# Optimization experiments

Measured on AMD Instinct MI355X. Metric: run time of the kernel, lower is better.

Reference implementation:

```python
import jax, jax.numpy as jnp
import numpy as np

S_SIGMA = 8      # spatial downsampling of the bilateral grid
N_BINS = 16      # intensity bins (range resolution)
EPS = 1e-8


def _blur_axis(g, k, axis):
    """1D correlation of grid g with small tap filter k along `axis` (zero pad)."""
    taps = k.shape[0]
    r = taps // 2
    pad = [(0, 0)] * g.ndim
    pad[axis] = (r, r)
    gp = jnp.pad(g, pad)
    n = g.shape[axis]
    out = k[0] * jax.lax.slice_in_dim(gp, 0, n, axis=axis)
    for i in range(1, taps):
        out = out + k[i] * jax.lax.slice_in_dim(gp, i, i + n, axis=axis)
    return out


def _bilateral_one(img, fs, fr):
    """Bilateral grid splat -> blur -> slice for a single [H,W] channel.
    Guide signal is the channel itself (values assumed in [0,1])."""
    H, W = img.shape
    GH = (H - 1) // S_SIGMA + 2
    GW = (W - 1) // S_SIGMA + 2
    GZ = N_BINS + 1

    ys = jnp.arange(H, dtype=img.dtype)
    xs = jnp.arange(W, dtype=img.dtype)

    # ---- splat (nearest-cell scatter-add of homogeneous (value, weight)) ----
    gy = jnp.round(ys / S_SIGMA).astype(jnp.int32)            # [H]
    gx = jnp.round(xs / S_SIGMA).astype(jnp.int32)            # [W]
    gyg, gxg = jnp.meshgrid(gy, gx, indexing='ij')            # [H,W]
    gz = jnp.clip(jnp.round(img * (N_BINS - 1)), 0, N_BINS - 1).astype(jnp.int32)
    val = jnp.zeros((GH, GW, GZ), img.dtype).at[gyg, gxg, gz].add(img)
    wt = jnp.zeros((GH, GW, GZ), img.dtype).at[gyg, gxg, gz].add(jnp.ones_like(img))

    # ---- blur grid: learnable 5-tap filter_s along y,x and filter_r along z ----
    for axis, k in ((0, fs), (1, fs), (2, fr)):
        val = _blur_axis(val, k, axis)
        wt = _blur_axis(wt, k, axis)

    # ---- slice (trilinear gather at (y/s, x/s, I*(NB-1))) ----
    fy = ys / S_SIGMA
    fx = xs / S_SIGMA
    fz = jnp.clip(img * (N_BINS - 1), 0.0, N_BINS - 1)        # [H,W]
    y0 = jnp.floor(fy).astype(jnp.int32)
    x0 = jnp.floor(fx).astype(jnp.int32)
    z0 = jnp.floor(fz).astype(jnp.int32)
    y1 = jnp.minimum(y0 + 1, GH - 1)
    x1 = jnp.minimum(x0 + 1, GW - 1)
    z1 = jnp.minimum(z0 + 1, GZ - 1)
    ty = fy - y0.astype(img.dtype)                            # [H]
    tx = fx - x0.astype(img.dtype)                            # [W]
    tz = fz - z0.astype(img.dtype)                            # [H,W]

    out_v = jnp.zeros_like(img)
    out_w = jnp.zeros_like(img)
    for yi, wy in ((y0, 1.0 - ty), (y1, ty)):
        for xi, wx in ((x0, 1.0 - tx), (x1, tx)):
            for zi, wz in ((z0, 1.0 - tz), (z1, tz)):
                w = wy[:, None] * wx[None, :] * wz            # [H,W]
                out_v = out_v + w * val[yi[:, None], xi[None, :], zi]
                out_w = out_w + w * wt[yi[:, None], xi[None, :], zi]
    return out_v / (out_w + EPS)


def setup_inputs() -> dict:
    key = jax.random.key(0)
    k1, k2 = jax.random.split(key)
    blurred_batch = jax.random.uniform(k1, (4, 3, 1024, 1024), dtype=jnp.float32)
    kernel_batch = jax.random.uniform(k2, (4, 11, 11), dtype=jnp.float32)
    g = jnp.array([1.0, 4.0, 6.0, 4.0, 1.0], dtype=jnp.float32)
    g = g / g.sum()  # smooth 5-tap filter so the blur is nontrivial
    return {
        'blurred_batch': blurred_batch,
        'kernel_batch': kernel_batch,
        'filter_s': g,
        'filter_r': g,
        'num_irls_iter': 1,
        'num_cg_iter': 5,
    }


def reference(blurred_batch, kernel_batch, filter_s, filter_r, num_irls_iter, num_cg_iter):
    # kernel_batch, num_irls_iter, num_cg_iter are unused on this code path,
    # matching the original forward (only BilateralGrid.apply touches x).
    B, C, H, W = blurred_batch.shape
    imgs = blurred_batch.reshape(B * C, H, W)
    out = jax.vmap(lambda im: _bilateral_one(im, filter_s, filter_r))(imgs)
    return out.reshape(B, C, H, W)
```

## Files before the change

kernel.cpp:

```cpp
#include <hip/hip_runtime.h>

#define S_SIGMA 8
#define NBINS   16
#define HDIM    1024
#define WDIM    1024
#define GH      129
#define GW      129
#define GZ      17
#define CELLS   (GH*GW*GZ)
#define ROWSZ   (GW*GZ)
#define EPSV    1e-8f
#define FIXS    1048576.0f
#define FIXI    (1.0f/1048576.0f)

__global__ __launch_bounds__(256) void splat_gather_kernel(
    const float* __restrict__ img, float* __restrict__ grid, int nImg, int imgBase)
{
    __shared__ unsigned lval[16 * 64];
    __shared__ unsigned lwt [16 * 64];

    int tid = threadIdx.x;
    int c   = tid & 63;
    int q   = tid >> 6;
    int cellIdx = blockIdx.x * 64 + c;
    int total = nImg * GH * GW;

    for (int i = tid; i < 16 * 64; i += 256) { lval[i] = 0u; lwt[i] = 0u; }
    __syncthreads();

    if (cellIdx < total) {
        int b   = cellIdx / (GH * GW);
        int rem = cellIdx - b * (GH * GW);
        int gy  = rem / GW;
        int gx  = rem - gy * GW;
        const float* ib = img + (size_t)(imgBase + b) * (HDIM * WDIM);

        bool interior = (gx >= 1) & (gx <= 127) & (gy >= 1) & (gy <= 127);
        if (interior) {
            int py = gy & 1, px = gx & 1;
            int ylo = 8 * gy - 4 + py;
            int nr  = 9 - 2 * py;
            int ax  = 8 * gx - 4;
            for (int r = q; r < nr; r += 4) {
                const float* rp = ib + (size_t)(ylo + r) * WDIM + ax;
                float4 A = *(const float4*)rp;
                float4 B = *(const float4*)(rp + 4);
                float  cv = rp[8];
                float e7[7] = {A.y, A.z, A.w, B.x, B.y, B.z, B.w};
                #pragma unroll
                for (int j = 0; j < 7; ++j) {
                    float v = e7[j];
                    int gz = min(max((int)rintf(v * 15.0f), 0), 15);
                    atomicAdd(&lval[gz * 64 + c], (unsigned)rintf(v * FIXS));
                    atomicAdd(&lwt [gz * 64 + c], 1u);
                }
                if (!px) {
                    int gz = min(max((int)rintf(A.x * 15.0f), 0), 15);
                    atomicAdd(&lval[gz * 64 + c], (unsigned)rintf(A.x * FIXS));
                    atomicAdd(&lwt [gz * 64 + c], 1u);
                    gz = min(max((int)rintf(cv * 15.0f), 0), 15);
                    atomicAdd(&lval[gz * 64 + c], (unsigned)rintf(cv * FIXS));
                    atomicAdd(&lwt [gz * 64 + c], 1u);
                }
            }
        } else {
            int ylo = max(0, 8 * gy - 4 + (gy & 1));
            int yhi = min(HDIM - 1, 8 * gy + 4 - (gy & 1));
            int xlo = max(0, 8 * gx - 4 + (gx & 1));
            int xhi = min(WDIM - 1, 8 * gx + 4 - (gx & 1));
            for (int y = ylo + q; y <= yhi; y += 4) {
                const float* row = ib + (size_t)y * WDIM;
                for (int x = xlo; x <= xhi; ++x) {
                    float v = row[x];
                    int gz = min(max((int)rintf(v * 15.0f), 0), 15);
                    atomicAdd(&lval[gz * 64 + c], (unsigned)rintf(v * FIXS));
                    atomicAdd(&lwt [gz * 64 + c], 1u);
                }
            }
        }
    }
    __syncthreads();

    if (cellIdx < total) {
        float2* dst = (float2*)grid + (size_t)cellIdx * GZ;
        int zlo = q * 4;
        int zhi = (q == 3) ? 17 : zlo + 4;
        for (int z = zlo; z < zhi; ++z) {
            float2 o;
            if (z == 16) { o.x = 0.f; o.y = 0.f; }
            else {
                o.x = (float)lval[z * 64 + c] * FIXI;
                o.y = (float)lwt [z * 64 + c];
            }
            dst[z] = o;
        }
    }
}

#define TO 12
#define TI 16
#define NIN  (TI*TI*GZ)
#define NTMP (TO*TI*GZ)
#define NOUT (TO*TO*GZ)
#define NTI  13
#define NXI  10

__global__ __launch_bounds__(256) void blur_fused_kernel(
    const float2* __restrict__ in, float2* __restrict__ out,
    const float* __restrict__ kfs, const float* __restrict__ kfr)
{
    __shared__ float2 sbin[NIN];

    int tid = threadIdx.x;
    int tx0 = blockIdx.x * TO;
    int ty0 = blockIdx.y * TO;
    int b   = blockIdx.z;

    float ks[5] = {kfs[0], kfs[1], kfs[2], kfs[3], kfs[4]};
    float kr[5] = {kfr[0], kfr[1], kfr[2], kfr[3], kfr[4]};

    const float2* gb = in + (size_t)b * CELLS;
    for (int li = tid; li < NIN; li += 256) {
        int iy = li / (TI * GZ);
        int r  = li - iy * (TI * GZ);
        int ix = r / GZ;
        int z  = r - ix * GZ;
        int gy = ty0 - 2 + iy;
        int gx = tx0 - 2 + ix;
        float2 v; v.x = 0.f; v.y = 0.f;
        if (gy >= 0 && gy < GH && gx >= 0 && gx < GW)
            v = gb[((size_t)gy * GW + gx) * GZ + z];
        sbin[li] = v;
    }
    __syncthreads();

    float2 rt[NTI];
    #pragma unroll
    for (int it = 0; it < NTI; ++it) {
        int o = tid + it * 256;
        float2 a; a.x = 0.f; a.y = 0.f;
        if (o < NTMP) {
            int oy = o / (TI * GZ);
            int r  = o - oy * (TI * GZ);
            #pragma unroll
            for (int t = 0; t < 5; ++t) {
                float2 g = sbin[(oy + t) * (TI * GZ) + r];
                a.x += ks[t] * g.x;
                a.y += ks[t] * g.y;
            }
        }
        rt[it] = a;
    }
    __syncthreads();
    #pragma unroll
    for (int it = 0; it < NTI; ++it) {
        int o = tid + it * 256;
        if (o < NTMP) sbin[o] = rt[it];
    }
    __syncthreads();

    float2 rx[NXI];
    #pragma unroll
    for (int it = 0; it < NXI; ++it) {
        int o = tid + it * 256;
        float2 a; a.x = 0.f; a.y = 0.f;
        if (o < NOUT) {
            int oy = o / (TO * GZ);
            int r  = o - oy * (TO * GZ);
            int ox = r / GZ;
            int z  = r - ox * GZ;
            #pragma unroll
            for (int t = 0; t < 5; ++t) {
                float2 g = sbin[(oy * TI + ox + t) * GZ + z];
                a.x += ks[t] * g.x;
                a.y += ks[t] * g.y;
            }
        }
        rx[it] = a;
    }
    __syncthreads();
    #pragma unroll
    for (int it = 0; it < NXI; ++it) {
        int o = tid + it * 256;
        if (o < NOUT) sbin[o] = rx[it];
    }
    __syncthreads();

    float2* ob = out + (size_t)b * CELLS;
    for (int o = tid; o < NOUT; o += 256) {
        int oy = o / (GZ * TO);
        int r2 = o - oy * (GZ * TO);
        int z  = r2 / TO;
        int ox = r2 - z * TO;
        int gy = ty0 + oy;
        int gx = tx0 + ox;
        if (gy < GH && gx < GW) {
            int cb = (oy * TO + ox) * GZ;
            float2 a; a.x = 0.f; a.y = 0.f;
            #pragma unroll
            for (int t = 0; t < 5; ++t) {
                int zz = z + t - 2;
                if (zz >= 0 && zz < GZ) {
                    float2 g = sbin[cb + zz];
                    a.x += kr[t] * g.x;
                    a.y += kr[t] * g.y;
                }
            }
            ob[((size_t)gy * GZ + z) * GW + gx] = a;
        }
    }
}

#define XP2   136
#define RST   XP2
#define ZST   (2*XP2)

__global__ __launch_bounds__(256) void slice_rows_kernel(
    const float* __restrict__ img, const float2* __restrict__ grid,
    float* __restrict__ out, int imgBase)
{
    __shared__ float2 sg[GZ * ZST];

    int tid = threadIdx.x;
    int k   = blockIdx.x;
    int b   = blockIdx.y;

    const float2* gsrc = grid + (size_t)b * CELLS + (size_t)k * ROWSZ;
    for (int i = tid; i < 2 * ROWSZ; i += 256) {
        int r   = i / ROWSZ;
        int rem = i - r * ROWSZ;
        int z   = rem / GW;
        int x0  = rem - z * GW;
        sg[z * ZST + r * RST + x0] = gsrc[i];
    }
    __syncthreads();

    int x   = tid << 2;
    int x0v = tid >> 1;
    float txb = (float)(x & 7) * 0.125f;

    size_t rowBase = (size_t)(imgBase + b) * (HDIM * WDIM) + (size_t)(k << 3) * WDIM + x;

    #pragma unroll
    for (int r = 0; r < 8; ++r) {
        size_t pixBase = rowBase + (size_t)r * WDIM;
        float4 v4 = *(const float4*)(img + pixBase);
        float ty = (float)r * 0.125f;
        float wy0 = 1.f - ty, wy1 = ty;

        float vv[4] = {v4.x, v4.y, v4.z, v4.w};
        float rr[4];
        #pragma unroll
        for (int j = 0; j < 4; ++j) {
            float v  = vv[j];
            float fz = fminf(fmaxf(v * 15.0f, 0.0f), 15.0f);
            float zf = floorf(fz);
            int   z0 = (int)zf;
            float tz = fz - zf;
            float tx = txb + (float)j * 0.125f;
            float wx0 = 1.f - tx, wx1 = tx;
            float wz0 = 1.f - tz, wz1 = tz;

            int base = z0 * ZST + x0v;
            float2 g000 = sg[base];
            float2 g010 = sg[base + 1];
            float2 g100 = sg[base + RST];
            float2 g110 = sg[base + RST + 1];
            float2 g001 = sg[base + ZST];
            float2 g011 = sg[base + ZST + 1];
            float2 g101 = sg[base + ZST + RST];
            float2 g111 = sg[base + ZST + RST + 1];

            float ov = 0.f, ow = 0.f, w;
            w = wy0 * wx0 * wz0; ov += w * g000.x; ow += w * g000.y;
            w = wy0 * wx0 * wz1; ov += w * g001.x; ow += w * g001.y;
            w = wy0 * wx1 * wz0; ov += w * g010.x; ow += w * g010.y;
            w = wy0 * wx1 * wz1; ov += w * g011.x; ow += w * g011.y;
            w = wy1 * wx0 * wz0; ov += w * g100.x; ow += w * g100.y;
            w = wy1 * wx0 * wz1; ov += w * g101.x; ow += w * g101.y;
            w = wy1 * wx1 * wz0; ov += w * g110.x; ow += w * g110.y;
            w = wy1 * wx1 * wz1; ov += w * g111.x; ow += w * g111.y;
            rr[j] = ov / (ow + EPSV);
        }
        float4 r4; r4.x = rr[0]; r4.y = rr[1]; r4.z = rr[2]; r4.w = rr[3];
        *(float4*)(out + pixBase) = r4;
    }
}

extern "C" void kernel_launch(void* const* d_in, const int* in_sizes, int n_in,
                              void* d_out, int out_size, void* d_ws, size_t ws_size,
                              hipStream_t stream)
{
    const float* img = (const float*)d_in[0];
    const float* fs  = (const float*)d_in[2];
    const float* fr  = (const float*)d_in[3];
    float* out = (float*)d_out;

    int nImgTotal = in_sizes[0] / (HDIM * WDIM);
    size_t perImgBytes = (size_t)CELLS * 2 * sizeof(float);

    int maxChunk = (int)(ws_size / (2 * perImgBytes));
    if (maxChunk < 1) return;
    if (maxChunk > nImgTotal) maxChunk = nImgTotal;

    const int tilesPerDim = (GH + TO - 1) / TO;

    for (int base = 0; base < nImgTotal; base += maxChunk) {
        int c = nImgTotal - base;
        if (c > maxChunk) c = maxChunk;

        float* A = (float*)d_ws;
        float* B = A + (size_t)c * CELLS * 2;

        int nCells = c * GH * GW;
        int cellBlocks = (nCells + 63) / 64;
        splat_gather_kernel<<<cellBlocks, 256, 0, stream>>>(img, A, c, base);

        dim3 bgrid(tilesPerDim, tilesPerDim, c);
        blur_fused_kernel<<<bgrid, 256, 0, stream>>>((const float2*)A, (float2*)B, fs, fr);

        dim3 sgrid(HDIM / 8, c);
        slice_rows_kernel<<<sgrid, 256, 0, stream>>>(img, (const float2*)B, out, base);
    }
}
```

Before: 93.43 us.

## Split fused grid blur into two z-halves to shrink LDS per block

The fused y/x/z blur kernel is templated on a z-half. Each launch loads 11 of the 17 z-bins (with halo) and writes 9 or 8 output bins, so shared memory and register arrays shrink, and launch bounds now request higher occupancy. The cost is two launches and about 30% redundant halo loads and y/x blur work on the overlapping z bins.

After: 98.14 us. 1.05x slower.

```diff
diff --git a/kernel.cpp b/kernel.cpp
--- a/kernel.cpp
+++ b/kernel.cpp
@@ -12,6 +12,7 @@
 #define EPSV    1e-8f
 #define FIXS    1048576.0f
 #define FIXI    (1.0f/1048576.0f)
+
 
 __global__ __launch_bounds__(256) void splat_gather_kernel(
     const float* __restrict__ img, float* __restrict__ grid, int nImg, int imgBase)
@@ -99,17 +100,24 @@
 
 #define TO 12
 #define TI 16
-#define NIN  (TI*TI*GZ)
-#define NTMP (TO*TI*GZ)
-#define NOUT (TO*TO*GZ)
-#define NTI  13
-#define NXI  10
-
-__global__ __launch_bounds__(256) void blur_fused_kernel(
+
+template <int H>
+__global__ __launch_bounds__(256, 6) void blur_fused_kernel(
     const float2* __restrict__ in, float2* __restrict__ out,
     const float* __restrict__ kfs, const float* __restrict__ kfr)
 {
-    __shared__ float2 sbin[NIN];
+    constexpr int ZB  = H * 7;
+    constexpr int NZI = 11 - H;
+    constexpr int NZO = 9 - H;
+    constexpr int ZOL = 9 * H;
+    constexpr int NIN  = TI * TI * NZI;
+    constexpr int NTMP = TO * TI * NZI;
+    constexpr int NX   = TO * TO * NZI;
+    constexpr int NOUT = TO * TO * NZO;
+    constexpr int NTI  = (NTMP + 255) / 256;
+    constexpr int NXI  = (NX   + 255) / 256;
+
+    __shared__ float2 sbin[TI * TI * 11];
 
     int tid = threadIdx.x;
     int tx0 = blockIdx.x * TO;
@@ -121,15 +129,15 @@
 
     const float2* gb = in + (size_t)b * CELLS;
     for (int li = tid; li < NIN; li += 256) {
-        int iy = li / (TI * GZ);
-        int r  = li - iy * (TI * GZ);
-        int ix = r / GZ;
-        int z  = r - ix * GZ;
+        int iy = li / (TI * NZI);
+        int r  = li - iy * (TI * NZI);
+        int ix = r / NZI;
+        int zi = r - ix * NZI;
         int gy = ty0 - 2 + iy;
         int gx = tx0 - 2 + ix;
         float2 v; v.x = 0.f; v.y = 0.f;
         if (gy >= 0 && gy < GH && gx >= 0 && gx < GW)
-            v = gb[((size_t)gy * GW + gx) * GZ + z];
+            v = gb[((size_t)gy * GW + gx) * GZ + ZB + zi];
         sbin[li] = v;
     }
     __syncthreads();
@@ -140,11 +148,11 @@
         int o = tid + it * 256;
         float2 a; a.x = 0.f; a.y = 0.f;
         if (o < NTMP) {
-            int oy = o / (TI * GZ);
-            int r  = o - oy * (TI * GZ);
+            int oy = o / (TI * NZI);
+            int r  = o - oy * (TI * NZI);
             #pragma unroll
             for (int t = 0; t < 5; ++t) {
-                float2 g = sbin[(oy + t) * (TI * GZ) + r];
+                float2 g = sbin[(oy + t) * (TI * NZI) + r];
                 a.x += ks[t] * g.x;
                 a.y += ks[t] * g.y;
             }
@@ -164,14 +172,14 @@
     for (int it = 0; it < NXI; ++it) {
         int o = tid + it * 256;
         float2 a; a.x = 0.f; a.y = 0.f;
-        if (o < NOUT) {
-            int oy = o / (TO * GZ);
-            int r  = o - oy * (TO * GZ);
-            int ox = r / GZ;
-            int z  = r - ox * GZ;
+        if (o < NX) {
+            int oy = o / (TO * NZI);
+            int r  = o - oy * (TO * NZI);
+            int ox = r / NZI;
+            int zi = r - ox * NZI;
             #pragma unroll
             for (int t = 0; t < 5; ++t) {
-                float2 g = sbin[(oy * TI + ox + t) * GZ + z];
+                float2 g = sbin[oy * (TI * NZI) + (ox + t) * NZI + zi];
                 a.x += ks[t] * g.x;
                 a.y += ks[t] * g.y;
             }
@@ -182,31 +190,32 @@
     #pragma unroll
     for (int it = 0; it < NXI; ++it) {
         int o = tid + it * 256;
-        if (o < NOUT) sbin[o] = rx[it];
+        if (o < NX) sbin[o] = rx[it];
     }
     __syncthreads();
 
     float2* ob = out + (size_t)b * CELLS;
     for (int o = tid; o < NOUT; o += 256) {
-        int oy = o / (GZ * TO);
-        int r2 = o - oy * (GZ * TO);
-        int z  = r2 / TO;
-        int ox = r2 - z * TO;
+        int oy = o / (NZO * TO);
+        int r2 = o - oy * (NZO * TO);
+        int k  = r2 / TO;
+        int ox = r2 - k * TO;
+        int zo = ZOL + k;
         int gy = ty0 + oy;
         int gx = tx0 + ox;
         if (gy < GH && gx < GW) {
-            int cb = (oy * TO + ox) * GZ;
+            int cb = (oy * TO + ox) * NZI;
             float2 a; a.x = 0.f; a.y = 0.f;
             #pragma unroll
             for (int t = 0; t < 5; ++t) {
-                int zz = z + t - 2;
-                if (zz >= 0 && zz < GZ) {
-                    float2 g = sbin[cb + zz];
+                int zg = zo + t - 2;
+                if (zg >= 0 && zg <= 16) {
+                    float2 g = sbin[cb + zg - ZB];
                     a.x += kr[t] * g.x;
                     a.y += kr[t] * g.y;
                 }
             }
-            ob[((size_t)gy * GZ + z) * GW + gx] = a;
+            ob[((size_t)gy * GZ + zo) * GW + gx] = a;
         }
     }
 }
@@ -317,7 +326,8 @@
         splat_gather_kernel<<<cellBlocks, 256, 0, stream>>>(img, A, c, base);
 
         dim3 bgrid(tilesPerDim, tilesPerDim, c);
-        blur_fused_kernel<<<bgrid, 256, 0, stream>>>((const float2*)A, (float2*)B, fs, fr);
+        blur_fused_kernel<0><<<bgrid, 256, 0, stream>>>((const float2*)A, (float2*)B, fs, fr);
+        blur_fused_kernel<1><<<bgrid, 256, 0, stream>>>((const float2*)A, (float2*)B, fs, fr);
 
         dim3 sgrid(HDIM / 8, c);
         slice_rows_kernel<<<sgrid, 256, 0, stream>>>(img, (const float2*)B, out, base);
```
